# Kernel optimization log

Measured on AMD Instinct MI355X. Metric: run time of the kernel, lower is better.

The kernel has to match this reference:

```python
import jax, jax.numpy as jnp
import numpy as np

N_E = 1024      # nconcepts (codebook size)
E_DIM = 64      # cdim (codebook vector dim)
BETA = 0.25
LEGACY = True


def setup_inputs() -> dict:
    key = jax.random.key(0)
    k1, k2, k3 = jax.random.split(key, 3)
    z_ = jax.random.normal(k1, (32, 256, 32, 32), jnp.float32)
    # 1x1 conv dis_modulator: 256 -> 64 channels (stored as [out, in])
    conv_w = jax.random.normal(k2, (64, 256), jnp.float32) / np.sqrt(256.0)
    conv_b = jnp.zeros((64,), jnp.float32)
    # embedding.weight.data.uniform_(-1/n_e, 1/n_e)
    emb = jax.random.uniform(k3, (N_E, E_DIM), jnp.float32, -1.0 / N_E, 1.0 / N_E)
    return {"z_": z_, "conv_w": conv_w, "conv_b": conv_b, "emb": emb}


def _forward(z_, conv_w, conv_b, emb):
    sg = jax.lax.stop_gradient
    # dis_modulator: 1x1 conv == per-pixel linear map  (B,Cin,H,W)->(B,Cout,H,W)
    z = jnp.einsum('bchw,oc->bohw', z_, conv_w) + conv_b[None, :, None, None]
    B = z.shape[0]
    # torch .view(-1, e_dim): row-major flatten of (B,C,H,W) into chunks of e_dim
    zf = z.reshape(-1, E_DIM)  # [B*C*H*W/e_dim, e_dim]

    # contrastive term: mean pairwise cosine similarity of codebook rows
    d1 = emb @ emb.T                                  # [n_e, n_e]
    norms = jnp.linalg.norm(emb, axis=1)              # [n_e]
    cosine = d1 / (norms[:, None] * norms[None, :])
    contrastive = jnp.mean(cosine)

    # squared L2 distances: ||z||^2 + ||e||^2 - 2 z.e
    d = (jnp.sum(zf * zf, axis=1, keepdims=True)
         + jnp.sum(emb * emb, axis=1)[None, :]
         - 2.0 * (zf @ emb.T))                        # [N, n_e]
    idx = jnp.argmin(d, axis=1)                       # [N]
    z_q = emb[idx].reshape(z.shape)

    if LEGACY:
        loss = jnp.mean((sg(z_q) - z) ** 2) + BETA * jnp.mean((z_q - sg(z)) ** 2)
    else:
        loss = BETA * jnp.mean((sg(z_q) - z) ** 2) + jnp.mean((z_q - sg(z)) ** 2)
    # hessian_penalty(G, z_, G_z=z): G is an affine 1x1 conv, so the central
    # second difference G(z+x) - 2G(z) + G(z-x) is identically zero -> penalty = 0.
    loss = loss + contrastive

    # straight-through estimator
    z_q_st = z + sg(z_q - z)

    # replicate source exactly: flat zeros(B*n_e) scattered at codebook indices
    sampled = jnp.zeros((B * N_E,), z.dtype).at[idx].set(1.0).reshape(B, N_E)
    min_idx = idx.reshape(B, -1)
    return z_q_st, loss, sampled, min_idx


def reference(z_, conv_w, conv_b, emb):
    z_q, loss, sampled, min_idx = _forward(z_, conv_w, conv_b, emb)
    return z_q, loss, sampled, min_idx
```

## Files before the change

kernel.cpp:

```cpp
#include <hip/hip_runtime.h>

#define BATCH   32
#define CIN     256
#define COUT    64
#define HW      1024
#define NE      1024
#define ED      64
#define NROW    32768
#define ZTOT    2097152

#define OFF_LOSS 2097152
#define OFF_SAMP 2097153
#define OFF_IDX  2129921

#define CXSTR 68
#define ZKSTR 68
#define EKSTR 260

__global__ __launch_bounds__(256, 4) void k_pre(const float* __restrict__ x,
                                                const float* __restrict__ w,
                                                const float* __restrict__ bias,
                                                float* __restrict__ z,
                                                const float* __restrict__ emb,
                                                float* __restrict__ out_samp,
                                                float* __restrict__ enorm,
                                                float* __restrict__ cpart,
                                                unsigned int* __restrict__ counter) {
    __shared__ float SH[64 * CXSTR * 2];
    int bx = blockIdx.x;
    int t  = threadIdx.x;

    if (bx < 512) {
        float* Xs = SH;
        float* Ws = SH + 64 * CXSTR;
        int b  = bx >> 4;
        int p0 = (bx & 15) * 64;
        int pg = t & 15;
        int og = t >> 4;
        float acc[4][4];
        #pragma unroll
        for (int i = 0; i < 4; i++)
            #pragma unroll
            for (int j = 0; j < 4; j++) acc[i][j] = 0.0f;

        for (int c0 = 0; c0 < CIN; c0 += 64) {
            __syncthreads();
            {
                int u = t & 15, cg2 = t >> 4;
                #pragma unroll
                for (int m = 0; m < 4; m++) {
                    int c = cg2 + 16 * m;
                    float4 v = *(const float4*)&x[(size_t)(b * CIN + c0 + c) * HW + p0 + 4 * u];
                    *(float4*)&Xs[c * CXSTR + 4 * u] = v;
                }
                #pragma unroll
                for (int m = 0; m < 4; m++) {
                    int o = cg2 + 16 * m;
                    float4 v = *(const float4*)&w[o * CIN + c0 + 4 * u];
                    Ws[(4 * u + 0) * CXSTR + o] = v.x;
                    Ws[(4 * u + 1) * CXSTR + o] = v.y;
                    Ws[(4 * u + 2) * CXSTR + o] = v.z;
                    Ws[(4 * u + 3) * CXSTR + o] = v.w;
                }
            }
            __syncthreads();
            #pragma unroll 8
            for (int k = 0; k < 64; k++) {
                float4 xv = *(const float4*)&Xs[k * CXSTR + 4 * pg];
                float4 wv = *(const float4*)&Ws[k * CXSTR + 4 * og];
                float xa[4] = {xv.x, xv.y, xv.z, xv.w};
                float wb[4] = {wv.x, wv.y, wv.z, wv.w};
                #pragma unroll
                for (int i = 0; i < 4; i++)
                    #pragma unroll
                    for (int j = 0; j < 4; j++)
                        acc[i][j] = fmaf(xa[i], wb[j], acc[i][j]);
            }
        }
        #pragma unroll
        for (int j = 0; j < 4; j++) {
            int o = 4 * og + j;
            float bv = bias[o];
            float4 out;
            out.x = acc[0][j] + bv;
            out.y = acc[1][j] + bv;
            out.z = acc[2][j] + bv;
            out.w = acc[3][j] + bv;
            *(float4*)&z[(size_t)(b * COUT + o) * HW + p0 + 4 * pg] = out;
        }
        return;
    }
    if (bx < 640) {
        if (bx == 512 && t == 0) *counter = 0u;
        out_samp[(bx - 512) * 256 + t] = 0.0f;
        return;
    }
    if (bx < 656) {
        float* invl = SH;
        float* S    = SH + 64;
        int b2 = bx - 640;
        int i0 = b2 * 64;
        if (t < 64) {
            const float* e = emb + (size_t)(i0 + t) * ED;
            float r8[8];
            #pragma unroll
            for (int s = 0; s < 8; s++) { float xx = e[s]; r8[s] = xx * xx; }
            #pragma unroll
            for (int m = 1; m < 8; m++) {
                #pragma unroll
                for (int s = 0; s < 8; s++) { float xx = e[8 * m + s]; r8[s] += xx * xx; }
            }
            float en = ((r8[0] + r8[1]) + (r8[2] + r8[3])) + ((r8[4] + r8[5]) + (r8[6] + r8[7]));
            invl[t] = 1.0f / sqrtf(en);
        }
        __syncthreads();
        int d = t & 63, q = t >> 6;
        float s = 0.0f;
        #pragma unroll
        for (int m = 0; m < 16; m++) {
            int il = q + 4 * m;
            s = fmaf(emb[(size_t)(i0 + il) * ED + d], invl[il], s);
        }
        S[t] = s;
        __syncthreads();
        if (t < 64)
            cpart[b2 * 64 + t] = (S[t] + S[t + 64]) + (S[t + 128] + S[t + 192]);
        return;
    }
    {
        int j = (bx - 656) * 256 + t;
        const float* e = emb + (size_t)j * ED;
        float r8[8];
        #pragma unroll
        for (int s = 0; s < 8; s++) { float xx = e[s]; r8[s] = xx * xx; }
        #pragma unroll
        for (int m = 1; m < 8; m++) {
            #pragma unroll
            for (int s = 0; s < 8; s++) { float xx = e[8 * m + s]; r8[s] += xx * xx; }
        }
        enorm[j] = ((r8[0] + r8[1]) + (r8[2] + r8[3])) + ((r8[4] + r8[5]) + (r8[6] + r8[7]));
    }
}

__global__ __launch_bounds__(256, 2) void k_dist(const float* __restrict__ z,
                                                 const float* __restrict__ emb,
                                                 const float* __restrict__ enorm,
                                                 const float* __restrict__ cpart,
                                                 float* __restrict__ out_idx,
                                                 float* __restrict__ out_samp,
                                                 float* __restrict__ out_zq,
                                                 float* __restrict__ ssep,
                                                 float* __restrict__ out_loss,
                                                 unsigned int* __restrict__ counter) {
    __shared__ float zs[64 * ZKSTR];
    __shared__ float es[32 * EKSTR];
    __shared__ float zn_s[64];
    __shared__ float en_s[256];
    __shared__ float warr[4];
    __shared__ int   lastflag;
    __shared__ float CS;
    float* redd_s = es;
    int*   redj_s = (int*)(es + 2048);
    int*   bj_s   = (int*)(es + 4096);
    int t = threadIdx.x;
    int row0 = blockIdx.x * 64;
    int rg = t & 7;
    int cg = t >> 3;

    {
        int k = t & 63, wv = t >> 6;
        #pragma unroll
        for (int m = 0; m < 4; m++) {
            int v = wv + 4 * m;
            float4 val;
            val.x = z[(size_t)(row0 + 4 * v + 0) * ED + k];
            val.y = z[(size_t)(row0 + 4 * v + 1) * ED + k];
            val.z = z[(size_t)(row0 + 4 * v + 2) * ED + k];
            val.w = z[(size_t)(row0 + 4 * v + 3) * ED + k];
            *(float4*)&zs[k * ZKSTR + 4 * v] = val;
        }
    }
    if (t < 64) {
        const float* zr = z + (size_t)(row0 + t) * ED;
        float r8[8];
        #pragma unroll
        for (int s = 0; s < 8; s++) { float xx = zr[s]; r8[s] = xx * xx; }
        #pragma unroll
        for (int m = 1; m < 8; m++) {
            #pragma unroll
            for (int s = 0; s < 8; s++) { float xx = zr[8 * m + s]; r8[s] += xx * xx; }
        }
        zn_s[t] = ((r8[0] + r8[1]) + (r8[2] + r8[3])) + ((r8[4] + r8[5]) + (r8[6] + r8[7]));
    }

    float bestd[8];
    int   bestj[8];
    #pragma unroll
    for (int i = 0; i < 8; i++) { bestd[i] = __builtin_huge_valf(); bestj[i] = 0; }

    for (int ch = 0; ch < 4; ch++) {
        int c0 = ch * 256;
        float acc[8][8];
        #pragma unroll
        for (int i = 0; i < 8; i++)
            #pragma unroll
            for (int j = 0; j < 8; j++) acc[i][j] = 0.0f;

        for (int kh = 0; kh < 2; kh++) {
            int kb = kh * 32;
            __syncthreads();
            {
                int k = t & 31, wv = t >> 5;
                #pragma unroll
                for (int m = 0; m < 8; m++) {
                    int v = wv + 8 * m;
                    float4 val;
                    val.x = emb[(size_t)(c0 + 4 * v + 0) * ED + kb + k];
                    val.y = emb[(size_t)(c0 + 4 * v + 1) * ED + kb + k];
                    val.z = emb[(size_t)(c0 + 4 * v + 2) * ED + kb + k];
                    val.w = emb[(size_t)(c0 + 4 * v + 3) * ED + kb + k];
                    *(float4*)&es[k * EKSTR + 4 * v] = val;
                }
                if (kh == 0 && t < 64) {
                    float4 ev = *(const float4*)&enorm[c0 + 4 * t];
                    *(float4*)&en_s[4 * t] = ev;
                }
            }
            __syncthreads();

            #pragma unroll 4
            for (int kk = 0; kk < 32; kk++) {
                float4 za0 = *(const float4*)&zs[(kb + kk) * ZKSTR + 8 * rg];
                float4 za1 = *(const float4*)&zs[(kb + kk) * ZKSTR + 8 * rg + 4];
                float4 eb0 = *(const float4*)&es[kk * EKSTR + 8 * cg];
                float4 eb1 = *(const float4*)&es[kk * EKSTR + 8 * cg + 4];
                float xa[8] = {za0.x, za0.y, za0.z, za0.w, za1.x, za1.y, za1.z, za1.w};
                float eb[8] = {eb0.x, eb0.y, eb0.z, eb0.w, eb1.x, eb1.y, eb1.z, eb1.w};
                #pragma unroll
                for (int i = 0; i < 8; i++)
                    #pragma unroll
                    for (int j = 0; j < 8; j++)
                        acc[i][j] = fmaf(xa[i], eb[j], acc[i][j]);
            }
        }

        #pragma unroll
        for (int i = 0; i < 8; i++) {
            float zn = zn_s[8 * rg + i];
            #pragma unroll
            for (int j = 0; j < 8; j++) {
                int cl = 8 * cg + j;
                float A = zn + en_s[cl];
                float D = A - 2.0f * acc[i][j];
                if (D < bestd[i]) { bestd[i] = D; bestj[i] = c0 + cl; }
            }
        }
    }

    __syncthreads();
    #pragma unroll
    for (int i = 0; i < 8; i++) {
        int rl = 8 * rg + i;
        redd_s[cg * 64 + rl] = bestd[i];
        redj_s[cg * 64 + rl] = bestj[i];
    }
    __syncthreads();
    if (t < 64) {
        float bd = __builtin_huge_valf();
        int   bj = 0x7fffffff;
        #pragma unroll
        for (int c = 0; c < 32; c++) {
            float dd = redd_s[c * 64 + t];
            int   jj = redj_s[c * 64 + t];
            if (dd < bd || (dd == bd && jj < bj)) { bd = dd; bj = jj; }
        }
        int rowg = row0 + t;
        bj_s[t]       = bj;
        out_idx[rowg] = (float)bj;
        atomicExch(&out_samp[bj], 1.0f);
    }
    __syncthreads();

    {
        int r  = t & 63;
        int kq = t >> 6;
        int bj = bj_s[r];
        const float* er = emb + (size_t)bj * ED + kq * 16;
        float sq = 0.0f;
        #pragma unroll
        for (int m = 0; m < 4; m++) {
            float4 ev = *(const float4*)&er[4 * m];
            int kk = kq * 16 + 4 * m;
            float zv0 = zs[(kk + 0) * ZKSTR + r];
            float zv1 = zs[(kk + 1) * ZKSTR + r];
            float zv2 = zs[(kk + 2) * ZKSTR + r];
            float zv3 = zs[(kk + 3) * ZKSTR + r];
            float d0 = ev.x - zv0, d1 = ev.y - zv1, d2 = ev.z - zv2, d3 = ev.w - zv3;
            float4 o4;
            o4.x = zv0 + d0; o4.y = zv1 + d1; o4.z = zv2 + d2; o4.w = zv3 + d3;
            *(float4*)&out_zq[(size_t)(row0 + r) * ED + kk] = o4;
            sq += d0 * d0; sq += d1 * d1; sq += d2 * d2; sq += d3 * d3;
        }
        #pragma unroll
        for (int off = 32; off > 0; off >>= 1) sq += __shfl_down(sq, off, 64);
        if ((t & 63) == 0) warr[t >> 6] = sq;
    }
    __syncthreads();

    if (t == 0) {
        ssep[blockIdx.x] = (warr[0] + warr[1]) + (warr[2] + warr[3]);
        __threadfence();
        unsigned int old = atomicAdd(counter, 1u);
        lastflag = (old == 511u) ? 1 : 0;
    }
    __syncthreads();
    if (lastflag) {
        __threadfence();
        double* SD = (double*)es;
        const volatile float* sv = (const volatile float*)ssep;
        SD[t] = (double)sv[t] + (double)sv[t + 256];
        __syncthreads();
        #pragma unroll
        for (int off = 128; off > 0; off >>= 1) {
            if (t < off) SD[t] += SD[t + off];
            __syncthreads();
        }
        if (t < 64) {
            float v = 0.0f;
            #pragma unroll
            for (int m = 0; m < 16; m++) v += cpart[m * 64 + t];
            float sq = v * v;
            #pragma unroll
            for (int off = 32; off > 0; off >>= 1) sq += __shfl_down(sq, off, 64);
            if (t == 0) CS = sq / (1024.0f * 1024.0f);
        }
        __syncthreads();
        if (t == 0) {
            float m = (float)(SD[0] / (double)ZTOT);
            float loss = m + 0.25f * m;
            out_loss[0] = loss + CS;
        }
    }
}

extern "C" void kernel_launch(void* const* d_in, const int* in_sizes, int n_in,
                              void* d_out, int out_size, void* d_ws, size_t ws_size,
                              hipStream_t stream) {
    (void)in_sizes; (void)n_in; (void)out_size; (void)ws_size;
    const float* z_     = (const float*)d_in[0];
    const float* conv_w = (const float*)d_in[1];
    const float* conv_b = (const float*)d_in[2];
    const float* emb    = (const float*)d_in[3];

    float* out      = (float*)d_out;
    float* out_zq   = out;
    float* out_loss = out + OFF_LOSS;
    float* out_samp = out + OFF_SAMP;
    float* out_idx  = out + OFF_IDX;

    char*  ws       = (char*)d_ws;
    float* wz       = (float*)ws;
    float* enorm    = (float*)(ws + 8388608);
    float* cpart    = (float*)(ws + 8392704);
    float* ssep     = (float*)(ws + 8396800);
    unsigned int* counter = (unsigned int*)(ws + 8398848);

    k_pre  <<<660, 256, 0, stream>>>(z_, conv_w, conv_b, wz, emb, out_samp, enorm, cpart, counter);
    k_dist <<<512, 256, 0, stream>>>(wz, emb, enorm, cpart, out_idx, out_samp, out_zq, ssep, out_loss, counter);
}
```

Before: 169.3 us.

## Retile distance kernel to 4x8 per-thread tiles over 128-code chunks

Changes the distance GEMM tiling in k_dist from 8x8 per-thread tiles over 256-code chunks (split into two K halves) to 4x8 tiles over 128-code chunks with the full K=64 staged at once. The reduction buffers get dedicated shared arrays instead of aliasing the embedding tile. The aim is lower register pressure and fewer per-chunk syncs, at the cost of a lower FMA-to-LDS-load ratio and more chunk iterations.

New measurement: 172.5 us. Within noise of the previous version (+1.9%).

```diff
diff --git a/kernel.cpp b/kernel.cpp
--- a/kernel.cpp
+++ b/kernel.cpp
@@ -6,7 +6,6 @@
 #define HW      1024
 #define NE      1024
 #define ED      64
-#define NROW    32768
 #define ZTOT    2097152
 
 #define OFF_LOSS 2097152
@@ -14,8 +13,8 @@
 #define OFF_IDX  2129921
 
 #define CXSTR 68
-#define ZKSTR 68
-#define EKSTR 260
+#define XSTR  68
+#define ESTR  132
 
 __global__ __launch_bounds__(256, 4) void k_pre(const float* __restrict__ x,
                                                 const float* __restrict__ w,
@@ -152,20 +151,21 @@
                                                  float* __restrict__ ssep,
                                                  float* __restrict__ out_loss,
                                                  unsigned int* __restrict__ counter) {
-    __shared__ float zs[64 * ZKSTR];
-    __shared__ float es[32 * EKSTR];
+    __shared__ float zs[64 * XSTR];
+    __shared__ float es[64 * ESTR];
     __shared__ float zn_s[64];
-    __shared__ float en_s[256];
+    __shared__ float en_s[128];
+    __shared__ float redd_s[16 * 64];
+    __shared__ int   redj_s[16 * 64];
+    __shared__ int   bj_s[64];
     __shared__ float warr[4];
+    __shared__ double SD[256];
     __shared__ int   lastflag;
     __shared__ float CS;
-    float* redd_s = es;
-    int*   redj_s = (int*)(es + 2048);
-    int*   bj_s   = (int*)(es + 4096);
     int t = threadIdx.x;
     int row0 = blockIdx.x * 64;
-    int rg = t & 7;
-    int cg = t >> 3;
+    int rg = t & 15;
+    int cg = t >> 4;
 
     {
         int k = t & 63, wv = t >> 6;
@@ -177,7 +177,7 @@
             val.y = z[(size_t)(row0 + 4 * v + 1) * ED + k];
             val.z = z[(size_t)(row0 + 4 * v + 2) * ED + k];
             val.w = z[(size_t)(row0 + 4 * v + 3) * ED + k];
-            *(float4*)&zs[k * ZKSTR + 4 * v] = val;
+            *(float4*)&zs[k * XSTR + 4 * v] = val;
         }
     }
     if (t < 64) {
@@ -193,60 +193,56 @@
         zn_s[t] = ((r8[0] + r8[1]) + (r8[2] + r8[3])) + ((r8[4] + r8[5]) + (r8[6] + r8[7]));
     }
 
-    float bestd[8];
-    int   bestj[8];
+    float bestd[4];
+    int   bestj[4];
     #pragma unroll
-    for (int i = 0; i < 8; i++) { bestd[i] = __builtin_huge_valf(); bestj[i] = 0; }
-
-    for (int ch = 0; ch < 4; ch++) {
-        int c0 = ch * 256;
-        float acc[8][8];
-        #pragma unroll
-        for (int i = 0; i < 8; i++)
+    for (int i = 0; i < 4; i++) { bestd[i] = __builtin_huge_valf(); bestj[i] = 0; }
+
+    for (int ch = 0; ch < 8; ch++) {
+        int c0 = ch * 128;
+        __syncthreads();
+        {
+            int k = t & 63, wv = t >> 6;
+            #pragma unroll
+            for (int m = 0; m < 8; m++) {
+                int v = wv + 4 * m;
+                float4 val;
+                val.x = emb[(size_t)(c0 + 4 * v + 0) * ED + k];
+                val.y = emb[(size_t)(c0 + 4 * v + 1) * ED + k];
+                val.z = emb[(size_t)(c0 + 4 * v + 2) * ED + k];
+                val.w = emb[(size_t)(c0 + 4 * v + 3) * ED + k];
+                *(float4*)&es[k * ESTR + 4 * v] = val;
+            }
+            if (t < 32) {
+                float4 ev4 = *(const float4*)&enorm[c0 + 4 * t];
+                *(float4*)&en_s[4 * t] = ev4;
+            }
+        }
+        __syncthreads();
+
+        float acc[4][8];
+        #pragma unroll
+        for (int i = 0; i < 4; i++)
             #pragma unroll
             for (int j = 0; j < 8; j++) acc[i][j] = 0.0f;
 
-        for (int kh = 0; kh < 2; kh++) {
-            int kb = kh * 32;
-            __syncthreads();
-            {
-                int k = t & 31, wv = t >> 5;
-                #pragma unroll
-                for (int m = 0; m < 8; m++) {
-                    int v = wv + 8 * m;
-                    float4 val;
-                    val.x = emb[(size_t)(c0 + 4 * v + 0) * ED + kb + k];
-                    val.y = emb[(size_t)(c0 + 4 * v + 1) * ED + kb + k];
-                    val.z = emb[(size_t)(c0 + 4 * v + 2) * ED + kb + k];
-                    val.w = emb[(size_t)(c0 + 4 * v + 3) * ED + kb + k];
-                    *(float4*)&es[k * EKSTR + 4 * v] = val;
-                }
-                if (kh == 0 && t < 64) {
-                    float4 ev = *(const float4*)&enorm[c0 + 4 * t];
-                    *(float4*)&en_s[4 * t] = ev;
-                }
-            }
-            __syncthreads();
-
-            #pragma unroll 4
-            for (int kk = 0; kk < 32; kk++) {
-                float4 za0 = *(const float4*)&zs[(kb + kk) * ZKSTR + 8 * rg];
-                float4 za1 = *(const float4*)&zs[(kb + kk) * ZKSTR + 8 * rg + 4];
-                float4 eb0 = *(const float4*)&es[kk * EKSTR + 8 * cg];
-                float4 eb1 = *(const float4*)&es[kk * EKSTR + 8 * cg + 4];
-                float xa[8] = {za0.x, za0.y, za0.z, za0.w, za1.x, za1.y, za1.z, za1.w};
-                float eb[8] = {eb0.x, eb0.y, eb0.z, eb0.w, eb1.x, eb1.y, eb1.z, eb1.w};
-                #pragma unroll
-                for (int i = 0; i < 8; i++)
-                    #pragma unroll
-                    for (int j = 0; j < 8; j++)
-                        acc[i][j] = fmaf(xa[i], eb[j], acc[i][j]);
-            }
-        }
-
-        #pragma unroll
-        for (int i = 0; i < 8; i++) {
-            float zn = zn_s[8 * rg + i];
+        #pragma unroll 8
+        for (int k = 0; k < 64; k++) {
+            float4 xv = *(const float4*)&zs[k * XSTR + 4 * rg];
+            float4 e0 = *(const float4*)&es[k * ESTR + 8 * cg];
+            float4 e1 = *(const float4*)&es[k * ESTR + 8 * cg + 4];
+            float xa[4] = {xv.x, xv.y, xv.z, xv.w};
+            float eb[8] = {e0.x, e0.y, e0.z, e0.w, e1.x, e1.y, e1.z, e1.w};
+            #pragma unroll
+            for (int i = 0; i < 4; i++)
+                #pragma unroll
+                for (int j = 0; j < 8; j++)
+                    acc[i][j] = fmaf(xa[i], eb[j], acc[i][j]);
+        }
+
+        #pragma unroll
+        for (int i = 0; i < 4; i++) {
+            float zn = zn_s[4 * rg + i];
             #pragma unroll
             for (int j = 0; j < 8; j++) {
                 int cl = 8 * cg + j;
@@ -257,19 +253,17 @@
         }
     }
 
-    __syncthreads();
     #pragma unroll
-    for (int i = 0; i < 8; i++) {
-        int rl = 8 * rg + i;
-        redd_s[cg * 64 + rl] = bestd[i];
-        redj_s[cg * 64 + rl] = bestj[i];
+    for (int i = 0; i < 4; i++) {
+        redd_s[cg * 64 + 4 * rg + i] = bestd[i];
+        redj_s[cg * 64 + 4 * rg + i] = bestj[i];
     }
     __syncthreads();
     if (t < 64) {
         float bd = __builtin_huge_valf();
         int   bj = 0x7fffffff;
         #pragma unroll
-        for (int c = 0; c < 32; c++) {
+        for (int c = 0; c < 16; c++) {
             float dd = redd_s[c * 64 + t];
             int   jj = redj_s[c * 64 + t];
             if (dd < bd || (dd == bd && jj < bj)) { bd = dd; bj = jj; }
@@ -290,20 +284,20 @@
         #pragma unroll
         for (int m = 0; m < 4; m++) {
             float4 ev = *(const float4*)&er[4 * m];
-            int kk = kq * 16 + 4 * m;
-            float zv0 = zs[(kk + 0) * ZKSTR + r];
-            float zv1 = zs[(kk + 1) * ZKSTR + r];
-            float zv2 = zs[(kk + 2) * ZKSTR + r];
-            float zv3 = zs[(kk + 3) * ZKSTR + r];
+            float zv0 = zs[(kq * 16 + 4 * m + 0) * XSTR + r];
+            float zv1 = zs[(kq * 16 + 4 * m + 1) * XSTR + r];
+            float zv2 = zs[(kq * 16 + 4 * m + 2) * XSTR + r];
+            float zv3 = zs[(kq * 16 + 4 * m + 3) * XSTR + r];
             float d0 = ev.x - zv0, d1 = ev.y - zv1, d2 = ev.z - zv2, d3 = ev.w - zv3;
             float4 o4;
             o4.x = zv0 + d0; o4.y = zv1 + d1; o4.z = zv2 + d2; o4.w = zv3 + d3;
-            *(float4*)&out_zq[(size_t)(row0 + r) * ED + kk] = o4;
+            *(float4*)&out_zq[(size_t)(row0 + r) * ED + kq * 16 + 4 * m] = o4;
             sq += d0 * d0; sq += d1 * d1; sq += d2 * d2; sq += d3 * d3;
         }
         #pragma unroll
         for (int off = 32; off > 0; off >>= 1) sq += __shfl_down(sq, off, 64);
-        if ((t & 63) == 0) warr[t >> 6] = sq;
+        int lane = t & 63, wv = t >> 6;
+        if (lane == 0) warr[wv] = sq;
     }
     __syncthreads();
 
@@ -316,7 +310,6 @@
     __syncthreads();
     if (lastflag) {
         __threadfence();
-        double* SD = (double*)es;
         const volatile float* sv = (const volatile float*)ssep;
         SD[t] = (double)sv[t] + (double)sv[t + 256];
         __syncthreads();
```
